# Optimization experiments

Hardware: AMD Instinct MI355X
Metric: run time of the kernel (lower is better)

Reference implementation:

```python
import jax, jax.numpy as jnp
import numpy as np
import math

EPS = 1e-07
ITERATIONS = 3
FINAL_LAMBDA = 0.01

B, H, W, K, CIN, COUT, P = 8, 12, 12, 3, 16, 32, 16


def setup_inputs() -> dict:
    key = jax.random.key(0)
    k1, k2, k3, k4 = jax.random.split(key, 4)
    V = jax.random.normal(k1, (B, H, W, K, K, CIN, COUT, P), dtype=jnp.float32)
    a = jax.random.uniform(k2, (B, H, W, K, K, CIN, 1), dtype=jnp.float32)
    Beta_u = jax.random.normal(k3, (1, 1, 1, 1, 1, 1, COUT, 1), dtype=jnp.float32)
    Beta_a = jax.random.normal(k4, (1, 1, 1, 1, 1, 1, COUT), dtype=jnp.float32)
    R = jnp.full((B, H, W, K, K, CIN, COUT), 1.0 / COUT, dtype=jnp.float32)
    outSize = (B, H, W, COUT, P)
    return {"V": V, "a": a, "Beta_u": Beta_u, "Beta_a": Beta_a, "R": R, "outSize": outSize}


def _l2_normalize(x, axis):
    n = jnp.sqrt(jnp.sum(x * x, axis=axis, keepdims=True))
    return x / jnp.maximum(n, 1e-12)  # matches F.normalize default eps


def reference(V, a, Beta_u, Beta_a, R, outSize):
    mathpilog = jnp.log(jnp.asarray(2.0 * math.pi, dtype=jnp.float32))
    mu = sigma_sqr = a_out = None
    for i in range(ITERATIONS):
        Lam = FINAL_LAMBDA * (1.0 - 0.95 ** (i + 1))
        Rw = (R * a)[..., None]                                  # [B,h,w,K,K,Cin,Cout,1]
        mu_denom = jnp.sum(Rw, axis=(3, 4, 5), keepdims=True)    # [B,h,w,1,1,1,Cout,1]
        mu = jnp.sum(Rw * V, axis=(3, 4, 5), keepdims=True) / (mu_denom + EPS)  # [B,h,w,1,1,1,Cout,P]
        V_mu_sqr = (V - mu) ** 2                                 # [B,h,w,K,K,Cin,Cout,P]
        sigma_sqr = jnp.sum(Rw * V_mu_sqr, axis=(3, 4, 5), keepdims=True) / (mu_denom + EPS)
        cost_h = (Beta_u + 0.5 * jnp.log(sigma_sqr)) * mu_denom  # [B,h,w,1,1,1,Cout,P]
        x = Lam * (Beta_a - jnp.sum(cost_h, axis=7))             # [B,h,w,1,1,1,Cout]
        a_out = jax.nn.sigmoid(_l2_normalize(x, axis=6))
        log_p1 = -0.5 * jnp.sum(mathpilog + jnp.log(sigma_sqr), axis=7) + EPS
        log_p2 = -jnp.sum(V_mu_sqr / (2.0 * sigma_sqr + EPS), axis=7)  # [B,h,w,K,K,Cin,Cout]
        R = jax.nn.softmax(jnp.log(a_out) + log_p1 + log_p2, axis=6)
    mu_out = jnp.squeeze(mu).reshape(outSize)
    sigma_out = jnp.squeeze(sigma_sqr).reshape(outSize)
    return mu_out, jnp.squeeze(a_out), sigma_out
```

## Files before the change

### kernel.cpp

```cpp
#include <hip/hip_runtime.h>
#include <math.h>

#define NPOS 1152
#define NN   144
#define COUT 32
#define PP   16
#define EPSF 1e-7f
#define LOG2PI 1.8378770664093453f

#define MU_OFF   0
#define A_OFF    589824
#define SIG_OFF  626688

__global__ void __launch_bounds__(256)
em_routing_kernel(const float* __restrict__ V,
                  const float* __restrict__ a,
                  const float* __restrict__ Bu,
                  const float* __restrict__ Ba,
                  const float* __restrict__ Rin,
                  float* __restrict__ out)
{
    const int pos  = blockIdx.x;
    const int tid  = threadIdx.x;
    const int c    = tid & 31;
    const int slot = tid >> 5;
    const int wave = tid >> 6;

    const float* Vp = V + (size_t)pos * (NN * COUT * PP);
    const float* Rp = Rin + (size_t)pos * (NN * COUT);

    __shared__ float a_s[NN];
    __shared__ float red[4][COUT][33];
    __shared__ float fin[COUT][33];
    __shared__ float mu_s[COUT][17];
    __shared__ float wp_s[COUT][17];
    __shared__ float sg_s[COUT][17];
    __shared__ float cl_s[COUT];
    __shared__ float xs[COUT];
    __shared__ float sl_s[COUT];
    __shared__ float ao_s[COUT];
    __shared__ float nrm_s;

    for (int i = tid; i < NN; i += 256) a_s[i] = a[pos * NN + i];
    __syncthreads();

    const float lam_tab[3] = {0.01f * (1.f - 0.95f),
                              0.01f * (1.f - 0.95f * 0.95f),
                              0.01f * (1.f - 0.95f * 0.95f * 0.95f)};

    float mu_r[PP], wp_r[PP];
    float cl_r = 0.f;

    for (int it = 0; it < 3; ++it) {
        if (it > 0) {
            #pragma unroll
            for (int p = 0; p < PP; ++p) {
                mu_r[p] = mu_s[c][p];
                wp_r[p] = wp_s[c][p];
            }
            cl_r = cl_s[c];
        }

        float S0 = 0.f, S1[PP], S2[PP];
        #pragma unroll
        for (int p = 0; p < PP; ++p) { S1[p] = 0.f; S2[p] = 0.f; }

        for (int j = 0; j < 18; ++j) {
            const int n = slot + (j << 3);
            const float4* vp = (const float4*)(Vp + (size_t)n * (COUT * PP) + c * PP);
            float4 q0 = vp[0], q1 = vp[1], q2 = vp[2], q3 = vp[3];
            float v[PP] = {q0.x,q0.y,q0.z,q0.w, q1.x,q1.y,q1.z,q1.w,
                           q2.x,q2.y,q2.z,q2.w, q3.x,q3.y,q3.z,q3.w};
            float Rw;
            if (it == 0) {
                Rw = Rp[n * COUT + c] * a_s[n];
            } else {
                float acc = 0.f;
                #pragma unroll
                for (int p = 0; p < PP; ++p) {
                    float d = v[p] - mu_r[p];
                    acc = fmaf(d * wp_r[p], d, acc);
                }
                float logit = cl_r - acc;
                float m = logit;
                #pragma unroll
                for (int msk = 1; msk <= 16; msk <<= 1)
                    m = fmaxf(m, __shfl_xor(m, msk, 64));
                float e = __expf(logit - m);
                float sum = e;
                #pragma unroll
                for (int msk = 1; msk <= 16; msk <<= 1)
                    sum += __shfl_xor(sum, msk, 64);
                Rw = (e / sum) * a_s[n];
            }
            S0 += Rw;
            #pragma unroll
            for (int p = 0; p < PP; ++p) {
                float t = Rw * v[p];
                S1[p] += t;
                S2[p] = fmaf(t, v[p], S2[p]);
            }
        }

        S0 += __shfl_xor(S0, 32, 64);
        #pragma unroll
        for (int p = 0; p < PP; ++p) {
            S1[p] += __shfl_xor(S1[p], 32, 64);
            S2[p] += __shfl_xor(S2[p], 32, 64);
        }
        if ((tid & 32) == 0) {
            red[wave][c][0] = S0;
            #pragma unroll
            for (int p = 0; p < PP; ++p) {
                red[wave][c][1 + p]  = S1[p];
                red[wave][c][17 + p] = S2[p];
            }
        }
        __syncthreads();
        for (int idx = tid; idx < COUT * 33; idx += 256) {
            int cc = idx / 33, k = idx - cc * 33;
            fin[cc][k] = red[0][cc][k] + red[1][cc][k] + red[2][cc][k] + red[3][cc][k];
        }
        __syncthreads();

        if (tid < COUT) {
            const int cc = tid;
            float d0  = fin[cc][0];
            float inv = 1.f / (d0 + EPSF);
            float sumlog = 0.f;
            #pragma unroll
            for (int p = 0; p < PP; ++p) {
                float s1 = fin[cc][1 + p];
                float s2 = fin[cc][17 + p];
                float mu = s1 * inv;
                float sg = (s2 - 2.f * mu * s1 + mu * mu * d0) * inv;
                sg = fmaxf(sg, 1e-30f);
                mu_s[cc][p] = mu;
                sg_s[cc][p] = sg;
                wp_s[cc][p] = 1.f / (2.f * sg + EPSF);
                sumlog += logf(sg);
            }
            sl_s[cc] = sumlog;
            xs[cc] = lam_tab[it] * (Ba[cc] - d0 * (16.f * Bu[cc] + 0.5f * sumlog));
        }
        __syncthreads();
        if (tid == 0) {
            float nn2 = 0.f;
            for (int cc = 0; cc < COUT; ++cc) nn2 += xs[cc] * xs[cc];
            nrm_s = sqrtf(nn2);
        }
        __syncthreads();
        if (tid < COUT) {
            const int cc = tid;
            float y  = xs[cc] / fmaxf(nrm_s, 1e-12f);
            float ao = 1.f / (1.f + expf(-y));
            ao_s[cc] = ao;
            cl_s[cc] = logf(ao) + (-0.5f * (16.f * LOG2PI + sl_s[cc]) + EPSF);
        }
        __syncthreads();
    }

    for (int idx = tid; idx < COUT * PP; idx += 256) {
        int cc = idx >> 4, p = idx & 15;
        out[MU_OFF  + (size_t)pos * (COUT * PP) + idx] = mu_s[cc][p];
        out[SIG_OFF + (size_t)pos * (COUT * PP) + idx] = sg_s[cc][p];
    }
    if (tid < COUT) out[A_OFF + pos * COUT + tid] = ao_s[tid];
}

extern "C" void kernel_launch(void* const* d_in, const int* in_sizes, int n_in,
                              void* d_out, int out_size, void* d_ws, size_t ws_size,
                              hipStream_t stream) {
    const float* V  = (const float*)d_in[0];
    const float* a  = (const float*)d_in[1];
    const float* Bu = (const float*)d_in[2];
    const float* Ba = (const float*)d_in[3];
    const float* R  = (const float*)d_in[4];
    float* out = (float*)d_out;
    em_routing_kernel<<<NPOS, 256, 0, stream>>>(V, a, Bu, Ba, R, out);
}
```

Measured before the change: 571.6 us.

## Replace shuffles with DPP reductions, redundantly compute per-capsule stats, prefetch V

```diff
diff --git a/kernel.cpp b/kernel.cpp
--- a/kernel.cpp
+++ b/kernel.cpp
@@ -12,7 +12,30 @@
 #define A_OFF    589824
 #define SIG_OFF  626688
 
-__global__ void __launch_bounds__(256)
+template<int CTRL>
+__device__ __forceinline__ float dppf(float x) {
+    return __int_as_float(__builtin_amdgcn_update_dpp(
+        0, __float_as_int(x), CTRL, 0xf, 0xf, true));
+}
+
+__device__ __forceinline__ float redmax32(float m) {
+    m = fmaxf(m, dppf<0xB1>(m));
+    m = fmaxf(m, dppf<0x4E>(m));
+    m = fmaxf(m, dppf<0x141>(m));
+    m = fmaxf(m, dppf<0x140>(m));
+    m = fmaxf(m, __shfl_xor(m, 16, 64));
+    return m;
+}
+__device__ __forceinline__ float redsum32(float s) {
+    s += dppf<0xB1>(s);
+    s += dppf<0x4E>(s);
+    s += dppf<0x141>(s);
+    s += dppf<0x140>(s);
+    s += __shfl_xor(s, 16, 64);
+    return s;
+}
+
+__global__ void __launch_bounds__(256, 4)
 em_routing_kernel(const float* __restrict__ V,
                   const float* __restrict__ a,
                   const float* __restrict__ Bu,
@@ -30,73 +53,68 @@
     const float* Rp = Rin + (size_t)pos * (NN * COUT);
 
     __shared__ float a_s[NN];
-    __shared__ float red[4][COUT][33];
-    __shared__ float fin[COUT][33];
-    __shared__ float mu_s[COUT][17];
-    __shared__ float wp_s[COUT][17];
-    __shared__ float sg_s[COUT][17];
-    __shared__ float cl_s[COUT];
-    __shared__ float xs[COUT];
-    __shared__ float sl_s[COUT];
-    __shared__ float ao_s[COUT];
-    __shared__ float nrm_s;
+    __shared__ __align__(16) float red[2][4][32][36];
 
     for (int i = tid; i < NN; i += 256) a_s[i] = a[pos * NN + i];
     __syncthreads();
 
-    const float lam_tab[3] = {0.01f * (1.f - 0.95f),
-                              0.01f * (1.f - 0.95f * 0.95f),
-                              0.01f * (1.f - 0.95f * 0.95f * 0.95f)};
-
-    float mu_r[PP], wp_r[PP];
-    float cl_r = 0.f;
-
+    const float Bu_c = Bu[c];
+    const float Ba_c = Ba[c];
+
+    float A_r[PP];
+    float B2_r[PP];
+    float cl2 = 0.f;
+    float mu[PP], sg[PP];
+    float ao = 0.f;
+
+    #pragma unroll
     for (int it = 0; it < 3; ++it) {
-        if (it > 0) {
-            #pragma unroll
-            for (int p = 0; p < PP; ++p) {
-                mu_r[p] = mu_s[c][p];
-                wp_r[p] = wp_s[c][p];
-            }
-            cl_r = cl_s[c];
-        }
+        const float lam = 0.01f * (1.f - ((it == 0) ? 0.95f
+                                         : (it == 1) ? 0.95f * 0.95f
+                                                     : 0.95f * 0.95f * 0.95f));
 
         float S0 = 0.f, S1[PP], S2[PP];
         #pragma unroll
         for (int p = 0; p < PP; ++p) { S1[p] = 0.f; S2[p] = 0.f; }
 
+        const float4* vq = (const float4*)(Vp + (size_t)slot * (COUT * PP) + c * PP);
+        const float*  rq = Rp + slot * COUT + c;
+
+        float4 n0 = vq[0], n1 = vq[1], n2 = vq[2], n3 = vq[3];
+        float  rv = (it == 0) ? *rq : 0.f;
+
+        #pragma unroll 1
         for (int j = 0; j < 18; ++j) {
-            const int n = slot + (j << 3);
-            const float4* vp = (const float4*)(Vp + (size_t)n * (COUT * PP) + c * PP);
-            float4 q0 = vp[0], q1 = vp[1], q2 = vp[2], q3 = vp[3];
-            float v[PP] = {q0.x,q0.y,q0.z,q0.w, q1.x,q1.y,q1.z,q1.w,
-                           q2.x,q2.y,q2.z,q2.w, q3.x,q3.y,q3.z,q3.w};
+            const float4 q0 = n0, q1 = n1, q2 = n2, q3 = n3;
+            const float  rc = rv;
+            if (j < 17) {
+                vq += 1024;
+                n0 = vq[0]; n1 = vq[1]; n2 = vq[2]; n3 = vq[3];
+                if (it == 0) { rq += 256; rv = *rq; }
+            }
+            const float av = a_s[slot + (j << 3)];
+
+            const float v[PP] = {q0.x,q0.y,q0.z,q0.w, q1.x,q1.y,q1.z,q1.w,
+                                 q2.x,q2.y,q2.z,q2.w, q3.x,q3.y,q3.z,q3.w};
             float Rw;
             if (it == 0) {
-                Rw = Rp[n * COUT + c] * a_s[n];
+                Rw = rc * av;
             } else {
-                float acc = 0.f;
+                float logit = cl2;
                 #pragma unroll
                 for (int p = 0; p < PP; ++p) {
-                    float d = v[p] - mu_r[p];
-                    acc = fmaf(d * wp_r[p], d, acc);
+                    const float t = fmaf(-A_r[p], v[p], B2_r[p]);
+                    logit = fmaf(t, v[p], logit);
                 }
-                float logit = cl_r - acc;
-                float m = logit;
-                #pragma unroll
-                for (int msk = 1; msk <= 16; msk <<= 1)
-                    m = fmaxf(m, __shfl_xor(m, msk, 64));
-                float e = __expf(logit - m);
-                float sum = e;
-                #pragma unroll
-                for (int msk = 1; msk <= 16; msk <<= 1)
-                    sum += __shfl_xor(sum, msk, 64);
-                Rw = (e / sum) * a_s[n];
+                const float m = redmax32(logit);
+                const float e = __expf(logit - m);
+                const float s = redsum32(e);
+                Rw = __fdividef(e, s) * av;
             }
             S0 += Rw;
             #pragma unroll
             for (int p = 0; p < PP; ++p) {
-                float t = Rw * v[p];
+                const float t = Rw * v[p];
                 S1[p] += t;
                 S2[p] = fmaf(t, v[p], S2[p]);
             }
@@ -108,64 +126,77 @@
             S1[p] += __shfl_xor(S1[p], 32, 64);
             S2[p] += __shfl_xor(S2[p], 32, 64);
         }
+
+        float* rb = &red[it & 1][wave][c][0];
         if ((tid & 32) == 0) {
-            red[wave][c][0] = S0;
-            #pragma unroll
-            for (int p = 0; p < PP; ++p) {
-                red[wave][c][1 + p]  = S1[p];
-                red[wave][c][17 + p] = S2[p];
-            }
+            #pragma unroll
+            for (int q = 0; q < 4; ++q)
+                ((float4*)rb)[q] = make_float4(S1[4*q], S1[4*q+1], S1[4*q+2], S1[4*q+3]);
+            rb[32] = S0;
+        } else {
+            #pragma unroll
+            for (int q = 0; q < 4; ++q)
+                ((float4*)rb)[4 + q] = make_float4(S2[4*q], S2[4*q+1], S2[4*q+2], S2[4*q+3]);
         }
         __syncthreads();
-        for (int idx = tid; idx < COUT * 33; idx += 256) {
-            int cc = idx / 33, k = idx - cc * 33;
-            fin[cc][k] = red[0][cc][k] + red[1][cc][k] + red[2][cc][k] + red[3][cc][k];
-        }
-        __syncthreads();
-
-        if (tid < COUT) {
-            const int cc = tid;
-            float d0  = fin[cc][0];
-            float inv = 1.f / (d0 + EPSF);
-            float sumlog = 0.f;
-            #pragma unroll
-            for (int p = 0; p < PP; ++p) {
-                float s1 = fin[cc][1 + p];
-                float s2 = fin[cc][17 + p];
-                float mu = s1 * inv;
-                float sg = (s2 - 2.f * mu * s1 + mu * mu * d0) * inv;
-                sg = fmaxf(sg, 1e-30f);
-                mu_s[cc][p] = mu;
-                sg_s[cc][p] = sg;
-                wp_s[cc][p] = 1.f / (2.f * sg + EPSF);
-                sumlog += logf(sg);
-            }
-            sl_s[cc] = sumlog;
-            xs[cc] = lam_tab[it] * (Ba[cc] - d0 * (16.f * Bu[cc] + 0.5f * sumlog));
-        }
-        __syncthreads();
-        if (tid == 0) {
-            float nn2 = 0.f;
-            for (int cc = 0; cc < COUT; ++cc) nn2 += xs[cc] * xs[cc];
-            nrm_s = sqrtf(nn2);
-        }
-        __syncthreads();
-        if (tid < COUT) {
-            const int cc = tid;
-            float y  = xs[cc] / fmaxf(nrm_s, 1e-12f);
-            float ao = 1.f / (1.f + expf(-y));
-            ao_s[cc] = ao;
-            cl_s[cc] = logf(ao) + (-0.5f * (16.f * LOG2PI + sl_s[cc]) + EPSF);
-        }
-        __syncthreads();
+
+        float s1[PP], s2[PP], d0 = 0.f;
+        #pragma unroll
+        for (int p = 0; p < PP; ++p) { s1[p] = 0.f; s2[p] = 0.f; }
+        #pragma unroll
+        for (int w = 0; w < 4; ++w) {
+            const float* rr = &red[it & 1][w][c][0];
+            #pragma unroll
+            for (int q = 0; q < 4; ++q) {
+                const float4 x = ((const float4*)rr)[q];
+                s1[4*q] += x.x; s1[4*q+1] += x.y; s1[4*q+2] += x.z; s1[4*q+3] += x.w;
+            }
+            #pragma unroll
+            for (int q = 0; q < 4; ++q) {
+                const float4 x = ((const float4*)rr)[4 + q];
+                s2[4*q] += x.x; s2[4*q+1] += x.y; s2[4*q+2] += x.z; s2[4*q+3] += x.w;
+            }
+            d0 += rr[32];
+        }
+
+        const float inv = __fdividef(1.f, d0 + EPSF);
+        float sumlog = 0.f;
+        #pragma unroll
+        for (int p = 0; p < PP; ++p) {
+            const float m_ = s1[p] * inv;
+            float g = (s2[p] - 2.f * m_ * s1[p] + m_ * m_ * d0) * inv;
+            g = fmaxf(g, 1e-30f);
+            mu[p] = m_;
+            sg[p] = g;
+            sumlog += __logf(g);
+        }
+        const float xs  = lam * (Ba_c - d0 * (16.f * Bu_c + 0.5f * sumlog));
+        const float nn2 = redsum32(xs * xs);
+        const float y   = xs / fmaxf(sqrtf(nn2), 1e-12f);
+        ao = 1.f / (1.f + __expf(-y));
+        const float cl = __logf(ao) - 0.5f * (16.f * LOG2PI + sumlog) + EPSF;
+
+        float Cacc = 0.f;
+        #pragma unroll
+        for (int p = 0; p < PP; ++p) {
+            const float wp = __fdividef(1.f, 2.f * sg[p] + EPSF);
+            A_r[p]  = wp;
+            B2_r[p] = 2.f * wp * mu[p];
+            Cacc = fmaf(wp * mu[p], mu[p], Cacc);
+        }
+        cl2 = cl - Cacc;
     }
 
-    for (int idx = tid; idx < COUT * PP; idx += 256) {
-        int cc = idx >> 4, p = idx & 15;
-        out[MU_OFF  + (size_t)pos * (COUT * PP) + idx] = mu_s[cc][p];
-        out[SIG_OFF + (size_t)pos * (COUT * PP) + idx] = sg_s[cc][p];
+    if (tid < 32) {
+        float4* mo = (float4*)(out + MU_OFF  + (size_t)pos * (COUT * PP) + c * PP);
+        float4* so = (float4*)(out + SIG_OFF + (size_t)pos * (COUT * PP) + c * PP);
+        #pragma unroll
+        for (int q = 0; q < 4; ++q) {
+            mo[q] = make_float4(mu[4*q], mu[4*q+1], mu[4*q+2], mu[4*q+3]);
+            so[q] = make_float4(sg[4*q], sg[4*q+1], sg[4*q+2], sg[4*q+3]);
+        }
+        out[A_OFF + pos * COUT + c] = ao;
     }
-    if (tid < COUT) out[A_OFF + pos * COUT + tid] = ao_s[tid];
 }
 
 extern "C" void kernel_launch(void* const* d_in, const int* in_sizes, int n_in,
```

Measured after the change: 558.7 us. 1.02x faster.
